# Kernel optimization log

Hardware: AMD Instinct MI355X
Metric: run time of the kernel (lower is better)

The kernel has to match this reference:

```python
import jax, jax.numpy as jnp
import numpy as np

C1, C2, K, S, P, D = 128, 128, 3, 1, 1, 1
B, H, W = 16, 64, 64
K2 = K * K


def conv2d(x, w, b=None, stride=1, pad=1, dil=1):
    y = jax.lax.conv_general_dilated(
        x, w, (stride, stride), [(pad, pad), (pad, pad)],
        rhs_dilation=(dil, dil), dimension_numbers=('NCHW', 'OIHW', 'NCHW'))
    if b is not None:
        y = y + b[None, :, None, None]
    return y


def setup_inputs() -> dict:
    key = jax.random.key(0)
    ks = jax.random.split(key, 6)
    fan = C1 * K * K
    x = jax.random.normal(ks[0], (B, C1, H, W), jnp.float32)
    w_conv = jax.random.normal(ks[1], (C2, C1, K, K), jnp.float32) / np.sqrt(fan)
    # small offset / mask branch weights -> realistic small learned offsets
    w_off = jax.random.normal(ks[2], (2 * K2, C1, K, K), jnp.float32) * 0.01
    b_off = jnp.zeros((2 * K2,), jnp.float32)
    w_mask = jax.random.normal(ks[3], (K2, C1, K, K), jnp.float32) * 0.01
    b_mask = jnp.zeros((K2,), jnp.float32)
    return {'x': x, 'w_conv': w_conv, 'w_off': w_off, 'b_off': b_off,
            'w_mask': w_mask, 'b_mask': b_mask}


def _deform_conv(x, offset, mask, w_conv):
    Bv, _, Hv, Wv = x.shape
    Ho, Wo = offset.shape[2], offset.shape[3]
    off = offset.reshape(Bv, K2, 2, Ho, Wo)
    off_y, off_x = off[:, :, 0], off[:, :, 1]
    # base sampling grid: out pixel + kernel tap (stride/pad/dilation)
    hs = (jnp.arange(Ho) * S - P).astype(jnp.float32)
    ws = (jnp.arange(Wo) * S - P).astype(jnp.float32)
    n = jnp.arange(K2)
    ky = ((n // K) * D).astype(jnp.float32)
    kx = ((n % K) * D).astype(jnp.float32)
    py = off_y + hs[None, None, :, None] + ky[None, :, None, None]  # [B,K2,Ho,Wo]
    px = off_x + ws[None, None, None, :] + kx[None, :, None, None]

    y0 = jnp.floor(py)
    x0 = jnp.floor(px)
    wy1 = py - y0
    wx1 = px - x0
    wy0 = 1.0 - wy1
    wx0 = 1.0 - wx1
    y0i = y0.astype(jnp.int32)
    x0i = x0.astype(jnp.int32)

    gather = jax.vmap(lambda xb, yi, xi: xb[:, yi, xi])  # -> [B,C,K2,Ho,Wo]

    def corner(yc, xc, wgt):
        valid = (yc >= 0) & (yc < Hv) & (xc >= 0) & (xc < Wv)
        yi = jnp.clip(yc, 0, Hv - 1)
        xi = jnp.clip(xc, 0, Wv - 1)
        v = gather(x, yi, xi)
        return v * (wgt * valid)[:, None]

    samp = (corner(y0i, x0i, wy0 * wx0)
            + corner(y0i, x0i + 1, wy0 * wx1)
            + corner(y0i + 1, x0i, wy1 * wx0)
            + corner(y0i + 1, x0i + 1, wy1 * wx1))  # [B,C1,K2,Ho,Wo]
    samp = samp * mask[:, None]
    wk = w_conv.reshape(C2, C1, K2)
    return jnp.einsum('bcnhw,ocn->bohw', samp, wk)


def reference(x, w_conv, w_off, b_off, w_mask, b_mask):
    offset = conv2d(x, w_off, b_off, S, P, D)
    mask = jax.nn.sigmoid(conv2d(x, w_mask, b_mask, S, P, D))
    return _deform_conv(x, offset, mask, w_conv)
```

## Files before the change

### kernel.cpp

```cpp
#include <hip/hip_runtime.h>
#include <math.h>

#define B_   16
#define C1_  128
#define C2_  128
#define H_   64
#define W_   64
#define HW_  4096
#define NCH_ 27

typedef __attribute__((ext_vector_type(8))) short  bf16x8;
typedef __attribute__((ext_vector_type(8))) unsigned short u16x8;
typedef __attribute__((ext_vector_type(4))) float  f32x4;
typedef __attribute__((ext_vector_type(4))) unsigned int u32x4;

__device__ __forceinline__ unsigned short f2bf(float f) {
  unsigned int u = __builtin_bit_cast(unsigned int, f);
  u += 0x7fff + ((u >> 16) & 1);
  return (unsigned short)(u >> 16);
}
__device__ __forceinline__ float lo16(unsigned int u) {
  return __builtin_bit_cast(float, u << 16);
}
__device__ __forceinline__ float hi16(unsigned int u) {
  return __builtin_bit_cast(float, u & 0xffff0000u);
}

__global__ __launch_bounds__(256) void xpose_k(const float* __restrict__ x,
                                               unsigned short* __restrict__ xcl) {
  __shared__ unsigned short tile[128][66];
  int bid = blockIdx.x;
  int bh = ((bid & 7) << 7) | (bid >> 3);
  int b = bh >> 6, h = bh & 63;
  int t = threadIdx.x;
  int wv = t & 63, cq = t >> 6;
  const float* xb = x + ((size_t)b * 128) * HW_ + h * 64;
#pragma unroll
  for (int i = 0; i < 32; ++i) {
    int c = i * 4 + cq;
    tile[c][wv] = f2bf(xb[(size_t)c * HW_ + wv]);
  }
  __syncthreads();
  int w2 = t >> 2, cg = (t & 3) * 32;
  unsigned short* op = xcl + (((size_t)bh) * 64 + w2) * 128 + cg;
#pragma unroll
  for (int i = 0; i < 4; ++i) {
    u16x8 pk;
#pragma unroll
    for (int j = 0; j < 8; ++j) pk[j] = tile[cg + i * 8 + j][w2];
    *reinterpret_cast<u16x8*>(op + i * 8) = pk;
  }
}

__global__ __launch_bounds__(256) void wpack_k(const float* __restrict__ wc,
                                               unsigned short* __restrict__ wpk) {
  int idx = blockIdx.x * 256 + threadIdx.x;
  if (idx >= 9 * 8 * 4 * 64 * 8) return;
  int j  = idx & 7;
  int l  = (idx >> 3) & 63;
  int kb = (idx >> 9) & 3;
  int ot = (idx >> 11) & 7;
  int n  = idx >> 14;
  int oc = ot * 16 + (l & 15);
  int c  = kb * 32 + (l >> 4) * 8 + j;
  wpk[idx] = f2bf(wc[(oc * 128 + c) * 9 + n]);
}

__global__ __launch_bounds__(256) void wobpack_k(const float* __restrict__ w_off,
                                                 const float* __restrict__ w_mask,
                                                 unsigned short* __restrict__ wob) {
  int idx = blockIdx.x * 256 + threadIdx.x;
  if (idx >= 2 * 36 * 64 * 8) return;
  int j = idx & 7;
  int l = (idx >> 3) & 63;
  int rest = idx >> 9;
  int s = rest % 36;
  int nt = rest / 36;
  int ch = nt * 16 + (l & 15);
  int n = s >> 2;
  int c = (s & 3) * 32 + (l >> 4) * 8 + j;
  float v = 0.f;
  if (ch < 18) v = w_off[((ch * 128) + c) * 9 + n];
  else if (ch < 27) v = w_mask[(((ch - 18) * 128) + c) * 9 + n];
  wob[idx] = f2bf(v);
}

__global__ __launch_bounds__(256) void offmask_k(
    const unsigned short* __restrict__ xcl,
    const unsigned short* __restrict__ wob,
    const float* __restrict__ b_off, const float* __restrict__ b_mask,
    float* __restrict__ om) {
  __shared__ __attribute__((aligned(16))) char xr[3 * 66 * 256];
  int bid = blockIdx.x;
  int bh = ((bid & 7) << 7) | (bid >> 3);
  int b = bh >> 6, h = bh & 63;
  int t = threadIdx.x;
  int l = t & 63, w = t >> 6;

#pragma unroll
  for (int ky = 0; ky < 3; ++ky) {
    int hh = h - 1 + ky;
    bool valid = (unsigned)hh < 64u;
    const unsigned short* src = xcl + (((size_t)b * 64 + (valid ? hh : 0)) * 64) * 128;
#pragma unroll
    for (int i = 0; i < 4; ++i) {
      int m = t + i * 256;
      int px = m >> 4;
      int c2 = (m & 15) * 16;
      unsigned off = (unsigned)((ky * 66 + px + 1) * 256 + c2) ^ (((px + 1) & 7) << 4);
      u16x8 v = {0, 0, 0, 0, 0, 0, 0, 0};
      if (valid) v = *reinterpret_cast<const u16x8*>(src + (size_t)m * 8);
      *reinterpret_cast<u16x8*>(xr + off) = v;
    }
  }
  if (t < 96) {
    int r = t >> 5, rem = t & 31;
    int slot = (rem < 16) ? 0 : 65;
    int c2 = (rem & 15) * 16;
    unsigned off = (unsigned)((r * 66 + slot) * 256 + c2) ^ ((slot & 7) << 4);
    u16x8 z = {0, 0, 0, 0, 0, 0, 0, 0};
    *reinterpret_cast<u16x8*>(xr + off) = z;
  }
  __syncthreads();

  f32x4 acc0 = (f32x4)0.f, acc1 = (f32x4)0.f;
#pragma unroll
  for (int n = 0; n < 9; ++n) {
    int ky = n / 3, kx = n % 3;
    int slot = w * 16 + (l & 15) + kx;
#pragma unroll
    for (int cs = 0; cs < 4; ++cs) {
      int s = n * 4 + cs;
      unsigned aoff = (unsigned)((ky * 66 + slot) * 256 + (l >> 4) * 16 + cs * 64)
                      ^ ((unsigned)(slot & 7) << 4);
      bf16x8 afr = *reinterpret_cast<const bf16x8*>(xr + aoff);
      bf16x8 bf0 = *reinterpret_cast<const bf16x8*>(wob + ((size_t)(0 * 36 + s) * 64 + l) * 8);
      bf16x8 bf1 = *reinterpret_cast<const bf16x8*>(wob + ((size_t)(1 * 36 + s) * 64 + l) * 8);
      acc0 = __builtin_amdgcn_mfma_f32_16x16x32_bf16(afr, bf0, acc0, 0, 0, 0);
      acc1 = __builtin_amdgcn_mfma_f32_16x16x32_bf16(afr, bf1, acc1, 0, 0, 0);
    }
  }

  int pxo = w * 16 + (l >> 4) * 4;
#pragma unroll
  for (int nt = 0; nt < 2; ++nt) {
    int ch = nt * 16 + (l & 15);
    f32x4 v = (nt == 0) ? acc0 : acc1;
    if (ch < 27) {
      float bias = (ch < 18) ? b_off[ch] : b_mask[ch - 18];
#pragma unroll
      for (int r = 0; r < 4; ++r) {
        float y = v[r] + bias;
        if (ch >= 18) y = 1.f / (1.f + __expf(-y));
        v[r] = y;
      }
      *reinterpret_cast<f32x4*>(om + ((size_t)b * NCH_ + ch) * HW_ + h * 64 + pxo) = v;
    }
  }
}

__device__ __forceinline__ bf16x8 blend4(u16x8 a, u16x8 b, u16x8 c, u16x8 d,
                                         float w0, float w1, float w2, float w3) {
  u32x4 ua = __builtin_bit_cast(u32x4, a);
  u32x4 ub = __builtin_bit_cast(u32x4, b);
  u32x4 uc = __builtin_bit_cast(u32x4, c);
  u32x4 ud = __builtin_bit_cast(u32x4, d);
  u32x4 r;
#pragma unroll
  for (int e = 0; e < 4; ++e) {
    float lo = w0 * lo16(ua[e]) + w1 * lo16(ub[e]) + w2 * lo16(uc[e]) + w3 * lo16(ud[e]);
    float hi = w0 * hi16(ua[e]) + w1 * hi16(ub[e]) + w2 * hi16(uc[e]) + w3 * hi16(ud[e]);
    unsigned ulo = __builtin_bit_cast(unsigned, lo) + 0x8000u;
    unsigned uhi = __builtin_bit_cast(unsigned, hi) + 0x8000u;
    r[e] = __builtin_amdgcn_perm(uhi, ulo, 0x07060302u);
  }
  return __builtin_bit_cast(bf16x8, r);
}

__global__ __launch_bounds__(512, 2) void dcn_k(
    const unsigned short* __restrict__ xcl,
    const unsigned short* __restrict__ wpk,
    const float* __restrict__ om,
    float* __restrict__ out) {
  __shared__ __attribute__((aligned(16))) unsigned short xrow[6 * 64 * 128];
  __shared__ __attribute__((aligned(16))) unsigned short wlds[16384];

  int bid = blockIdx.x;
  int bp = ((bid & 7) << 6) | (bid >> 3);
  int b = bp >> 5;
  int h0 = (bp & 31) * 2;
  int t = threadIdx.x;
  int l = t & 63;
  int w = t >> 6;
  int r = w >> 2;
  int q = w & 3;
  int h = h0 + r;

  const unsigned short* xb = xcl + ((size_t)b * HW_) * 128;
  const char* xbc = reinterpret_cast<const char*>(xb);

  int lo = max(0, h0 - 2), hi = min(63, h0 + 3);
  int nrows = hi - lo + 1;
  {
    const unsigned short* src = xb + ((size_t)lo * 64) * 128;
    int nchunks = nrows * 1024;
    for (int c = t; c < nchunks; c += 512) {
      int x = (c >> 4) & 63;
      unsigned dst = ((unsigned)c * 16) ^ (unsigned)((x & 7) << 4);
      *reinterpret_cast<u16x8*>(reinterpret_cast<char*>(xrow) + dst) =
          *reinterpret_cast<const u16x8*>(src + (size_t)c * 8);
    }
  }

  int px_l   = q * 16 + (l & 15);
  int cslice = (l >> 4) * 16;
  const float* ombr = om + (size_t)b * NCH_ * HW_ + h * 64;

  float omv[9][3];
#pragma unroll
  for (int n = 0; n < 9; ++n) {
    omv[n][0] = ombr[(2 * n) * HW_ + px_l];
    omv[n][1] = ombr[(2 * n + 1) * HW_ + px_l];
    omv[n][2] = ombr[(18 + n) * HW_ + px_l];
  }

  f32x4 acc[8];
#pragma unroll
  for (int t2 = 0; t2 < 8; ++t2) acc[t2] = (f32x4)0.f;

#pragma unroll
  for (int n = 0; n < 9; ++n) {
    const unsigned short* wsrc = wpk + (size_t)n * 16384 + t * 8;
    u16x8 wreg[4];
#pragma unroll
    for (int i = 0; i < 4; ++i)
      wreg[i] = *reinterpret_cast<const u16x8*>(wsrc + i * 4096);

    float oy = omv[n][0];
    float ox = omv[n][1];
    float m_ = omv[n][2];
    float py  = oy + (float)(h - 1 + n / 3);
    float pxf = ox + (float)(px_l - 1 + n % 3);
    float y0f = floorf(py), x0f = floorf(pxf);
    int y0 = (int)y0f, x0 = (int)x0f;
    float wy1 = py - y0f, wx1 = pxf - x0f;
    float wy0 = 1.f - wy1, wx0 = 1.f - wx1;
    bool vy0 = (unsigned)y0 < 64u, vy1 = (unsigned)(y0 + 1) < 64u;
    bool vx0 = (unsigned)x0 < 64u, vx1 = (unsigned)(x0 + 1) < 64u;
    int y0c = min(max(y0, 0), 63), y1c = min(max(y0 + 1, 0), 63);
    int x0c = min(max(x0, 0), 63), x1c = min(max(x0 + 1, 0), 63);
    float w00 = (vy0 && vx0) ? wy0 * wx0 * m_ : 0.f;
    float w01 = (vy0 && vx1) ? wy0 * wx1 * m_ : 0.f;
    float w10 = (vy1 && vx0) ? wy1 * wx0 * m_ : 0.f;
    float w11 = (vy1 && vx1) ? wy1 * wx1 * m_ : 0.f;

#pragma unroll
    for (int i = 0; i < 4; ++i)
      *reinterpret_cast<u16x8*>(wlds + t * 8 + i * 4096) = wreg[i];
    __syncthreads();

    bool inlds = ((unsigned)(y0c - lo) < (unsigned)nrows) &&
                 ((unsigned)(y1c - lo) < (unsigned)nrows);

    if (__all(inlds)) {
      int p00 = (y0c - lo) * 64 + x0c, p01 = (y0c - lo) * 64 + x1c;
      int p10 = (y1c - lo) * 64 + x0c, p11 = (y1c - lo) * 64 + x1c;
      unsigned s00 = (unsigned)((x0c & 7) << 4), s01 = (unsigned)((x1c & 7) << 4);
      const char* xr = reinterpret_cast<const char*>(xrow);
#pragma unroll
      for (int kb = 0; kb < 4; ++kb) {
        int cb = kb * 64 + cslice;
        u16x8 c0 = *reinterpret_cast<const u16x8*>(xr + (((unsigned)(p00 * 256 + cb)) ^ s00));
        u16x8 c1 = *reinterpret_cast<const u16x8*>(xr + (((unsigned)(p01 * 256 + cb)) ^ s01));
        u16x8 c2 = *reinterpret_cast<const u16x8*>(xr + (((unsigned)(p10 * 256 + cb)) ^ s00));
        u16x8 c3 = *reinterpret_cast<const u16x8*>(xr + (((unsigned)(p11 * 256 + cb)) ^ s01));
        bf16x8 afr = blend4(c0, c1, c2, c3, w00, w01, w10, w11);
#pragma unroll
        for (int t2 = 0; t2 < 8; ++t2) {
          bf16x8 bfr = *reinterpret_cast<const bf16x8*>(
              wlds + ((t2 * 4 + kb) * 64 + l) * 8);
          acc[t2] = __builtin_amdgcn_mfma_f32_16x16x32_bf16(afr, bfr, acc[t2], 0, 0, 0);
        }
      }
    } else {
      int i00 = (y0c * 64 + x0c) * 256, i01 = (y0c * 64 + x1c) * 256;
      int i10 = (y1c * 64 + x0c) * 256, i11 = (y1c * 64 + x1c) * 256;
#pragma unroll
      for (int kb = 0; kb < 4; ++kb) {
        int cb = kb * 64 + cslice;
        u16x8 c0 = *reinterpret_cast<const u16x8*>(xbc + i00 + cb);
        u16x8 c1 = *reinterpret_cast<const u16x8*>(xbc + i01 + cb);
        u16x8 c2 = *reinterpret_cast<const u16x8*>(xbc + i10 + cb);
        u16x8 c3 = *reinterpret_cast<const u16x8*>(xbc + i11 + cb);
        bf16x8 afr = blend4(c0, c1, c2, c3, w00, w01, w10, w11);
#pragma unroll
        for (int t2 = 0; t2 < 8; ++t2) {
          bf16x8 bfr = *reinterpret_cast<const bf16x8*>(
              wlds + ((t2 * 4 + kb) * 64 + l) * 8);
          acc[t2] = __builtin_amdgcn_mfma_f32_16x16x32_bf16(afr, bfr, acc[t2], 0, 0, 0);
        }
      }
    }
    __syncthreads();
  }

  int oc_l = l & 15;
  int px0 = q * 16 + (l >> 4) * 4;
#pragma unroll
  for (int t2 = 0; t2 < 8; ++t2) {
    int oc = t2 * 16 + oc_l;
    *reinterpret_cast<f32x4*>(out + ((size_t)b * C2_ + oc) * HW_ + h * 64 + px0) = acc[t2];
  }
}

extern "C" void kernel_launch(void* const* d_in, const int* in_sizes, int n_in,
                              void* d_out, int out_size, void* d_ws, size_t ws_size,
                              hipStream_t stream) {
  const float* x      = (const float*)d_in[0];
  const float* w_conv = (const float*)d_in[1];
  const float* w_off  = (const float*)d_in[2];
  const float* b_off  = (const float*)d_in[3];
  const float* w_mask = (const float*)d_in[4];
  const float* b_mask = (const float*)d_in[5];
  float* out = (float*)d_out;

  float* om = (float*)d_ws;
  unsigned short* wpk = (unsigned short*)(om + (size_t)B_ * NCH_ * HW_);
  unsigned short* wob = wpk + 147456;
  unsigned short* xcl = wob + 36864;

  hipLaunchKernelGGL(xpose_k, dim3(B_ * H_), dim3(256), 0, stream, x, xcl);
  hipLaunchKernelGGL(wpack_k, dim3(576), dim3(256), 0, stream, w_conv, wpk);
  hipLaunchKernelGGL(wobpack_k, dim3(144), dim3(256), 0, stream, w_off, w_mask, wob);
  hipLaunchKernelGGL(offmask_k, dim3(B_ * H_), dim3(256), 0, stream,
                     xcl, wob, b_off, b_mask, om);
  hipLaunchKernelGGL(dcn_k, dim3(512), dim3(512), 0, stream,
                     xcl, wpk, om, out);
}
```

Baseline: 92.73 us.

## Process four output rows per block with two pixel tiles per wave

Each block of the deformable conv kernel now covers 4 output rows instead of 2, and each wave handles two 16-pixel tiles, so the grid halves to 256 blocks. The change is meant to amortise each tap's weight tile loaded into LDS over twice as many pixels, and to share the staged input-row halo across more rows. In exchange it uses more LDS (8 rows staged) and more accumulator registers, allowing only 1 block per CU. With 256 blocks there may be fewer than one block per CU on a large GPU, which lowers occupancy and latency hiding.

```diff
diff --git a/kernel.cpp b/kernel.cpp
--- a/kernel.cpp
+++ b/kernel.cpp
@@ -177,29 +177,29 @@
   return __builtin_bit_cast(bf16x8, r);
 }
 
-__global__ __launch_bounds__(512, 2) void dcn_k(
+__global__ __launch_bounds__(512, 1) void dcn_k(
     const unsigned short* __restrict__ xcl,
     const unsigned short* __restrict__ wpk,
     const float* __restrict__ om,
     float* __restrict__ out) {
-  __shared__ __attribute__((aligned(16))) unsigned short xrow[6 * 64 * 128];
+  __shared__ __attribute__((aligned(16))) unsigned short xrow[8 * 64 * 128];
   __shared__ __attribute__((aligned(16))) unsigned short wlds[16384];
 
   int bid = blockIdx.x;
-  int bp = ((bid & 7) << 6) | (bid >> 3);
-  int b = bp >> 5;
-  int h0 = (bp & 31) * 2;
+  int bp = ((bid & 7) << 5) | (bid >> 3);
+  int b = bp >> 4;
+  int h0 = (bp & 15) * 4;
   int t = threadIdx.x;
   int l = t & 63;
   int w = t >> 6;
-  int r = w >> 2;
-  int q = w & 3;
-  int h = h0 + r;
+  int r2 = w >> 1;
+  int ph = w & 1;
+  int h = h0 + r2;
 
   const unsigned short* xb = xcl + ((size_t)b * HW_) * 128;
   const char* xbc = reinterpret_cast<const char*>(xb);
 
-  int lo = max(0, h0 - 2), hi = min(63, h0 + 3);
+  int lo = max(0, h0 - 2), hi = min(63, h0 + 5);
   int nrows = hi - lo + 1;
   {
     const unsigned short* src = xb + ((size_t)lo * 64) * 128;
@@ -212,21 +212,26 @@
     }
   }
 
-  int px_l   = q * 16 + (l & 15);
   int cslice = (l >> 4) * 16;
   const float* ombr = om + (size_t)b * NCH_ * HW_ + h * 64;
-
-  float omv[9][3];
-#pragma unroll
-  for (int n = 0; n < 9; ++n) {
-    omv[n][0] = ombr[(2 * n) * HW_ + px_l];
-    omv[n][1] = ombr[(2 * n + 1) * HW_ + px_l];
-    omv[n][2] = ombr[(18 + n) * HW_ + px_l];
-  }
-
-  f32x4 acc[8];
-#pragma unroll
-  for (int t2 = 0; t2 < 8; ++t2) acc[t2] = (f32x4)0.f;
+  int px0_l = ph * 32 + (l & 15);
+
+  float omv[9][2][3];
+#pragma unroll
+  for (int n = 0; n < 9; ++n)
+#pragma unroll
+    for (int m = 0; m < 2; ++m) {
+      int px = px0_l + m * 16;
+      omv[n][m][0] = ombr[(2 * n) * HW_ + px];
+      omv[n][m][1] = ombr[(2 * n + 1) * HW_ + px];
+      omv[n][m][2] = ombr[(18 + n) * HW_ + px];
+    }
+
+  f32x4 acc[2][8];
+#pragma unroll
+  for (int m = 0; m < 2; ++m)
+#pragma unroll
+    for (int t2 = 0; t2 < 8; ++t2) acc[m][t2] = (f32x4)0.f;
 
 #pragma unroll
   for (int n = 0; n < 9; ++n) {
@@ -235,81 +240,87 @@
 #pragma unroll
     for (int i = 0; i < 4; ++i)
       wreg[i] = *reinterpret_cast<const u16x8*>(wsrc + i * 4096);
-
-    float oy = omv[n][0];
-    float ox = omv[n][1];
-    float m_ = omv[n][2];
-    float py  = oy + (float)(h - 1 + n / 3);
-    float pxf = ox + (float)(px_l - 1 + n % 3);
-    float y0f = floorf(py), x0f = floorf(pxf);
-    int y0 = (int)y0f, x0 = (int)x0f;
-    float wy1 = py - y0f, wx1 = pxf - x0f;
-    float wy0 = 1.f - wy1, wx0 = 1.f - wx1;
-    bool vy0 = (unsigned)y0 < 64u, vy1 = (unsigned)(y0 + 1) < 64u;
-    bool vx0 = (unsigned)x0 < 64u, vx1 = (unsigned)(x0 + 1) < 64u;
-    int y0c = min(max(y0, 0), 63), y1c = min(max(y0 + 1, 0), 63);
-    int x0c = min(max(x0, 0), 63), x1c = min(max(x0 + 1, 0), 63);
-    float w00 = (vy0 && vx0) ? wy0 * wx0 * m_ : 0.f;
-    float w01 = (vy0 && vx1) ? wy0 * wx1 * m_ : 0.f;
-    float w10 = (vy1 && vx0) ? wy1 * wx0 * m_ : 0.f;
-    float w11 = (vy1 && vx1) ? wy1 * wx1 * m_ : 0.f;
-
 #pragma unroll
     for (int i = 0; i < 4; ++i)
       *reinterpret_cast<u16x8*>(wlds + t * 8 + i * 4096) = wreg[i];
     __syncthreads();
 
-    bool inlds = ((unsigned)(y0c - lo) < (unsigned)nrows) &&
-                 ((unsigned)(y1c - lo) < (unsigned)nrows);
-
-    if (__all(inlds)) {
-      int p00 = (y0c - lo) * 64 + x0c, p01 = (y0c - lo) * 64 + x1c;
-      int p10 = (y1c - lo) * 64 + x0c, p11 = (y1c - lo) * 64 + x1c;
-      unsigned s00 = (unsigned)((x0c & 7) << 4), s01 = (unsigned)((x1c & 7) << 4);
-      const char* xr = reinterpret_cast<const char*>(xrow);
-#pragma unroll
-      for (int kb = 0; kb < 4; ++kb) {
-        int cb = kb * 64 + cslice;
-        u16x8 c0 = *reinterpret_cast<const u16x8*>(xr + (((unsigned)(p00 * 256 + cb)) ^ s00));
-        u16x8 c1 = *reinterpret_cast<const u16x8*>(xr + (((unsigned)(p01 * 256 + cb)) ^ s01));
-        u16x8 c2 = *reinterpret_cast<const u16x8*>(xr + (((unsigned)(p10 * 256 + cb)) ^ s00));
-        u16x8 c3 = *reinterpret_cast<const u16x8*>(xr + (((unsigned)(p11 * 256 + cb)) ^ s01));
-        bf16x8 afr = blend4(c0, c1, c2, c3, w00, w01, w10, w11);
-#pragma unroll
-        for (int t2 = 0; t2 < 8; ++t2) {
-          bf16x8 bfr = *reinterpret_cast<const bf16x8*>(
-              wlds + ((t2 * 4 + kb) * 64 + l) * 8);
-          acc[t2] = __builtin_amdgcn_mfma_f32_16x16x32_bf16(afr, bfr, acc[t2], 0, 0, 0);
+#pragma unroll
+    for (int m = 0; m < 2; ++m) {
+      int px_l = px0_l + m * 16;
+      float oy = omv[n][m][0];
+      float ox = omv[n][m][1];
+      float m_ = omv[n][m][2];
+      float py  = oy + (float)(h - 1 + n / 3);
+      float pxf = ox + (float)(px_l - 1 + n % 3);
+      float y0f = floorf(py), x0f = floorf(pxf);
+      int y0 = (int)y0f, x0 = (int)x0f;
+      float wy1 = py - y0f, wx1 = pxf - x0f;
+      float wy0 = 1.f - wy1, wx0 = 1.f - wx1;
+      bool vy0 = (unsigned)y0 < 64u, vy1 = (unsigned)(y0 + 1) < 64u;
+      bool vx0 = (unsigned)x0 < 64u, vx1 = (unsigned)(x0 + 1) < 64u;
+      int y0c = min(max(y0, 0), 63), y1c = min(max(y0 + 1, 0), 63);
+      int x0c = min(max(x0, 0), 63), x1c = min(max(x0 + 1, 0), 63);
+      float w00 = (vy0 && vx0) ? wy0 * wx0 * m_ : 0.f;
+      float w01 = (vy0 && vx1) ? wy0 * wx1 * m_ : 0.f;
+      float w10 = (vy1 && vx0) ? wy1 * wx0 * m_ : 0.f;
+      float w11 = (vy1 && vx1) ? wy1 * wx1 * m_ : 0.f;
+
+      bool inlds = ((unsigned)(y0c - lo) < (unsigned)nrows) &&
+                   ((unsigned)(y1c - lo) < (unsigned)nrows);
+
+      if (__all(inlds)) {
+        int p00 = (y0c - lo) * 64 + x0c, p01 = (y0c - lo) * 64 + x1c;
+        int p10 = (y1c - lo) * 64 + x0c, p11 = (y1c - lo) * 64 + x1c;
+        unsigned s00 = (unsigned)((x0c & 7) << 4), s01 = (unsigned)((x1c & 7) << 4);
+        const char* xr = reinterpret_cast<const char*>(xrow);
+#pragma unroll
+        for (int kb = 0; kb < 4; ++kb) {
+          int cb = kb * 64 + cslice;
+          u16x8 c0 = *reinterpret_cast<const u16x8*>(xr + (((unsigned)(p00 * 256 + cb)) ^ s00));
+          u16x8 c1 = *reinterpret_cast<const u16x8*>(xr + (((unsigned)(p01 * 256 + cb)) ^ s01));
+          u16x8 c2 = *reinterpret_cast<const u16x8*>(xr + (((unsigned)(p10 * 256 + cb)) ^ s00));
+          u16x8 c3 = *reinterpret_cast<const u16x8*>(xr + (((unsigned)(p11 * 256 + cb)) ^ s01));
+          bf16x8 afr = blend4(c0, c1, c2, c3, w00, w01, w10, w11);
+#pragma unroll
+          for (int t2 = 0; t2 < 8; ++t2) {
+            bf16x8 bfr = *reinterpret_cast<const bf16x8*>(
+                wlds + ((t2 * 4 + kb) * 64 + l) * 8);
+            acc[m][t2] = __builtin_amdgcn_mfma_f32_16x16x32_bf16(afr, bfr, acc[m][t2], 0, 0, 0);
+          }
+        }
+      } else {
+        int i00 = (y0c * 64 + x0c) * 256, i01 = (y0c * 64 + x1c) * 256;
+        int i10 = (y1c * 64 + x0c) * 256, i11 = (y1c * 64 + x1c) * 256;
+#pragma unroll
+        for (int kb = 0; kb < 4; ++kb) {
+          int cb = kb * 64 + cslice;
+          u16x8 c0 = *reinterpret_cast<const u16x8*>(xbc + i00 + cb);
+          u16x8 c1 = *reinterpret_cast<const u16x8*>(xbc + i01 + cb);
+          u16x8 c2 = *reinterpret_cast<const u16x8*>(xbc + i10 + cb);
+          u16x8 c3 = *reinterpret_cast<const u16x8*>(xbc + i11 + cb);
+          bf16x8 afr = blend4(c0, c1, c2, c3, w00, w01, w10, w11);
+#pragma unroll
+          for (int t2 = 0; t2 < 8; ++t2) {
+            bf16x8 bfr = *reinterpret_cast<const bf16x8*>(
+                wlds + ((t2 * 4 + kb) * 64 + l) * 8);
+            acc[m][t2] = __builtin_amdgcn_mfma_f32_16x16x32_bf16(afr, bfr, acc[m][t2], 0, 0, 0);
+          }
         }
       }
-    } else {
-      int i00 = (y0c * 64 + x0c) * 256, i01 = (y0c * 64 + x1c) * 256;
-      int i10 = (y1c * 64 + x0c) * 256, i11 = (y1c * 64 + x1c) * 256;
-#pragma unroll
-      for (int kb = 0; kb < 4; ++kb) {
-        int cb = kb * 64 + cslice;
-        u16x8 c0 = *reinterpret_cast<const u16x8*>(xbc + i00 + cb);
-        u16x8 c1 = *reinterpret_cast<const u16x8*>(xbc + i01 + cb);
-        u16x8 c2 = *reinterpret_cast<const u16x8*>(xbc + i10 + cb);
-        u16x8 c3 = *reinterpret_cast<const u16x8*>(xbc + i11 + cb);
-        bf16x8 afr = blend4(c0, c1, c2, c3, w00, w01, w10, w11);
-#pragma unroll
-        for (int t2 = 0; t2 < 8; ++t2) {
-          bf16x8 bfr = *reinterpret_cast<const bf16x8*>(
-              wlds + ((t2 * 4 + kb) * 64 + l) * 8);
-          acc[t2] = __builtin_amdgcn_mfma_f32_16x16x32_bf16(afr, bfr, acc[t2], 0, 0, 0);
-        }
-      }
     }
     __syncthreads();
   }
 
   int oc_l = l & 15;
-  int px0 = q * 16 + (l >> 4) * 4;
-#pragma unroll
-  for (int t2 = 0; t2 < 8; ++t2) {
-    int oc = t2 * 16 + oc_l;
-    *reinterpret_cast<f32x4*>(out + ((size_t)b * C2_ + oc) * HW_ + h * 64 + px0) = acc[t2];
+#pragma unroll
+  for (int m = 0; m < 2; ++m) {
+    int px0 = ph * 32 + m * 16 + (l >> 4) * 4;
+#pragma unroll
+    for (int t2 = 0; t2 < 8; ++t2) {
+      int oc = t2 * 16 + oc_l;
+      *reinterpret_cast<f32x4*>(out + ((size_t)b * C2_ + oc) * HW_ + h * 64 + px0) = acc[m][t2];
+    }
   }
 }
 
@@ -334,6 +345,6 @@
   hipLaunchKernelGGL(wobpack_k, dim3(144), dim3(256), 0, stream, w_off, w_mask, wob);
   hipLaunchKernelGGL(offmask_k, dim3(B_ * H_), dim3(256), 0, stream,
                      xcl, wob, b_off, b_mask, om);
-  hipLaunchKernelGGL(dcn_k, dim3(512), dim3(512), 0, stream,
+  hipLaunchKernelGGL(dcn_k, dim3(256), dim3(512), 0, stream,
                      xcl, wpk, om, out);
 }
```

Result: slower. 97.50 us (+5.1%).
